# Kernel tuning notes

Measured on AMD Instinct MI355X. Metric: run time of the kernel, lower is better.

Reference implementation:

```python
import jax, jax.numpy as jnp
import numpy as np

B, T, D_MODEL, N_HEAD = 2, 2048, 1024, 16
HEAD_DIM = D_MODEL // N_HEAD
CHUNK, POLY = 16, 1
SCALE = HEAD_DIM ** -0.5


def alpert_basis(L):
    # poly_order=1: constant + linear Legendre-like columns, L2-normalized per column
    t = jnp.linspace(-1.0, 1.0, L)
    W = jnp.stack([jnp.ones_like(t), t], axis=1)  # [L, 2]
    return W / jnp.linalg.norm(W, axis=0, keepdims=True)


def setup_inputs() -> dict:
    key = jax.random.key(0)
    ks = jax.random.split(key, 10)
    d = D_MODEL
    nrm = lambda k, shape, s=0.02: (jax.random.normal(k, shape, jnp.float32) * s)
    return {
        'x': jax.random.normal(ks[0], (B, T, d), jnp.float32),
        'Wq': nrm(ks[1], (d, d)),
        'Wk': nrm(ks[2], (d, d)),
        'Wv': nrm(ks[3], (d, d)),
        'Wo': nrm(ks[4], (d, d)),
        'gate_w': nrm(ks[5], (d, d)),
        'gate_b': jnp.zeros((d,), jnp.float32),
        'A': nrm(ks[6], (N_HEAD, HEAD_DIM, HEAD_DIM)),
        'jump_scale': jnp.ones((1,), jnp.float32),
        'jump_bias': jnp.zeros((1,), jnp.float32),
        'sink_scalar': nrm(ks[7], (1, N_HEAD, 1, 1)),
        'v_null': nrm(ks[8], (1, N_HEAD, 1, HEAD_DIM)),
    }


def _forward(x, Wq, Wk, Wv, Wo, gate_w, gate_b, A, jump_scale, jump_bias, sink_scalar, v_null):
    Bx, Tx, C = x.shape
    H, Dh = N_HEAD, HEAD_DIM
    NEG = jnp.float32(-1e30)

    def lin(W):  # torch Linear: y = x @ W.T, W is [out, in]
        y = jnp.einsum('btc,dc->btd', x, W)
        return y.reshape(Bx, Tx, H, Dh).transpose(0, 2, 1, 3)  # [B,H,T,Dh]

    q_raw, k_raw, v_val = lin(Wq), lin(Wk), lin(Wv)
    g = jax.nn.sigmoid(jnp.einsum('btc,dc->btd', x, gate_w) + gate_b)
    gate = g.reshape(Bx, Tx, H, Dh).transpose(0, 2, 1, 3)

    # symmetric mean/std normalization (torch std is unbiased -> ddof=1)
    ms = 0.5 * (q_raw.mean(-1, keepdims=True) + k_raw.mean(-1, keepdims=True))
    ss = 0.5 * (jnp.std(q_raw, -1, keepdims=True, ddof=1) + jnp.std(k_raw, -1, keepdims=True, ddof=1))
    q_norm = (q_raw - ms) / (ss + 1e-6)
    k_norm = (k_raw - ms) / (ss + 1e-6)

    # RoPE (half-split variant as in source)
    inv = 1.0 / (10000.0 ** (jnp.arange(0, Dh, 2, dtype=jnp.float32) / Dh))
    fr = jnp.arange(Tx, dtype=jnp.float32)[:, None] * inv[None, :]  # [T, Dh/2]
    cos, sin = jnp.cos(fr)[None, None], jnp.sin(fr)[None, None]

    def rope(z):
        z1, z2 = z[..., 0::2], z[..., 1::2]
        return jnp.concatenate([-z2 * sin + z1 * cos, z1 * sin + z2 * cos], axis=-1)

    S = A - jnp.swapaxes(A, -1, -2)  # skew-symmetric per head
    wedge = lambda z: z + jnp.einsum('bhtd,hde->bhte', z, S)
    q_geo, k_geo = wedge(rope(q_norm)), wedge(rope(k_norm))

    W_b = alpert_basis(CHUNK)  # [L, K]
    N, K, L = Tx // CHUNK, W_b.shape[1], CHUNK
    to_chunks = lambda z: z.reshape(Bx, H, N, L, Dh).transpose(2, 0, 1, 3, 4)  # [N,B,H,L,Dh]
    qx, kx, gx = to_chunks(q_geo), to_chunks(k_geo), to_chunks(gate)

    hist0 = jnp.zeros((Bx, H, N, K, Dh), jnp.float32)
    last0 = jnp.zeros((Bx, H, 1, Dh), jnp.float32)
    idx = jnp.arange(N)

    def step(carry, xs):
        hist, last, i = carry
        q_c, k_c, g_c = xs  # [B,H,L,Dh]
        k_coef = jnp.einsum('bhld,lk->bhkd', k_c, W_b)
        sc = jnp.einsum('bhkd,bhnkd->bhn', k_coef, hist) * SCALE
        sc = jnp.where(idx < i, sc, NEG)  # mask unfilled history slots
        w = jax.nn.softmax(sc, axis=-1)
        retr = jnp.einsum('bhn,bhnkd->bhkd', w, hist)
        q_rec = jnp.einsum('bhkd,lk->bhld', retr, W_b)
        jg = jax.nn.sigmoid(sc.max(-1)[..., None, None] * jump_scale + jump_bias)  # [B,H,1,1]
        inj = jnp.where(i > 0, (1.0 - jg) * last + jg * q_rec, 0.0)
        q_out = jnp.cumsum(g_c * q_c, axis=2) + inj
        hist = hist.at[:, :, i].set(jnp.einsum('bhld,lk->bhkd', q_out, W_b))
        return (hist, q_out[:, :, -1:, :], i + 1), q_out

    _, q_outs = jax.lax.scan(step, (hist0, last0, jnp.int32(0)), (qx, kx, gx))
    Q = q_outs.transpose(1, 2, 0, 3, 4).reshape(Bx, H, Tx, Dh)

    att = jnp.einsum('bhtd,bhsd->bhts', Q, k_geo) * SCALE
    causal = jnp.tril(jnp.ones((Tx, Tx), bool))
    att = jnp.where(causal, att, NEG)
    null = jnp.broadcast_to(sink_scalar, (Bx, H, Tx, 1))
    probs = jax.nn.softmax(jnp.concatenate([att, null], axis=-1), axis=-1)
    out = jnp.einsum('bhts,bhsd->bhtd', probs[..., :Tx], v_val) + probs[..., Tx:] * v_null
    out = out.transpose(0, 2, 1, 3).reshape(Bx, Tx, C)
    return jnp.einsum('btc,dc->btd', out, Wo)


def reference(x, Wq, Wk, Wv, Wo, gate_w, gate_b, A, jump_scale, jump_bias, sink_scalar, v_null):
    return _forward(x, Wq, Wk, Wv, Wo, gate_w, gate_b, A, jump_scale, jump_bias, sink_scalar, v_null)
```

## Files before the change

### kernel.cpp

```cpp
#include <hip/hip_runtime.h>
#include <math.h>

#define NB 2
#define NT 2048
#define NH 16
#define DH 64
#define DM 1024

using bf8   = __attribute__((ext_vector_type(8))) short;
using f32x4 = __attribute__((ext_vector_type(4))) float;

static __device__ __forceinline__ ushort f2bf(float f) {
    union { float f; unsigned u; } c; c.f = f;
    unsigned u = c.u + 0x7FFFu + ((c.u >> 16) & 1u);
    return (ushort)(u >> 16);
}

static __device__ __forceinline__ float wbf(int l, int k) {
    if (k == 0) return 0.25f;
    const float invn = 1.0f / sqrtf(1360.0f / 225.0f);
    return (-1.0f + (2.0f / 15.0f) * (float)l) * invn;
}

__global__ __launch_bounds__(256) void cast3_kernel(
    const float* __restrict__ x, const float* __restrict__ wv,
    const float* __restrict__ wo, ushort* __restrict__ xb, ushort* __restrict__ wb)
{
    const int id = blockIdx.x * 256 + threadIdx.x;
    const int XQ = (NB * NT * DM) / 4;
    const int WQ = (DM * DM) / 4;
    const float4* src;
    ushort* dst;
    if (id < XQ) {
        src = (const float4*)x + id;
        dst = xb + (size_t)id * 4;
    } else {
        const int r = id - XQ;
        const int wi = r / WQ, off = r % WQ;
        const float* w = (wi == 0) ? wv : wo;
        src = (const float4*)w + off;
        dst = wb + (size_t)wi * DM * DM + (size_t)off * 4;
    }
    const float4 v = *src;
    ushort4 o;
    o.x = f2bf(v.x); o.y = f2bf(v.y); o.z = f2bf(v.z); o.w = f2bf(v.w);
    *(ushort4*)dst = o;
}

__global__ __launch_bounds__(512) void gemm3_f32_kernel(
    const float* __restrict__ x, const float* __restrict__ Wq,
    const float* __restrict__ Wk, const float* __restrict__ gw,
    const float* __restrict__ gbias,
    float* __restrict__ oq, float* __restrict__ ok, float* __restrict__ og)
{
    __shared__ float As[16][132];
    __shared__ float Bs[16][132];
    const int z = blockIdx.z;
    const float* Bw = (z == 0) ? Wq : (z == 1) ? Wk : gw;
    float* C = (z == 0) ? oq : (z == 1) ? ok : og;
    const int tid = threadIdx.x;
    const int tx = tid & 31;
    const int ty = tid >> 5;
    const int row0 = blockIdx.y * 128, col0 = blockIdx.x * 128;
    const int sr = tid >> 2;
    const int sk = (tid & 3) << 2;
    const float* Ap = x  + (size_t)(row0 + sr) * DM + sk;
    const float* Bp = Bw + (size_t)(col0 + sr) * DM + sk;
    float acc[8][4] = {};
    for (int k0 = 0; k0 < DM; k0 += 16) {
        const float4 av = *(const float4*)(Ap + k0);
        const float4 bv = *(const float4*)(Bp + k0);
        __syncthreads();
        As[sk + 0][sr] = av.x; As[sk + 1][sr] = av.y; As[sk + 2][sr] = av.z; As[sk + 3][sr] = av.w;
        Bs[sk + 0][sr] = bv.x; Bs[sk + 1][sr] = bv.y; Bs[sk + 2][sr] = bv.z; Bs[sk + 3][sr] = bv.w;
        __syncthreads();
        #pragma unroll
        for (int kk = 0; kk < 16; ++kk) {
            const float4 a0 = *(const float4*)&As[kk][ty * 4];
            const float4 a1 = *(const float4*)&As[kk][64 + ty * 4];
            const float4 b0 = *(const float4*)&Bs[kk][tx * 4];
            const float a[8] = {a0.x, a0.y, a0.z, a0.w, a1.x, a1.y, a1.z, a1.w};
            const float b[4] = {b0.x, b0.y, b0.z, b0.w};
            #pragma unroll
            for (int i = 0; i < 8; ++i)
                #pragma unroll
                for (int j = 0; j < 4; ++j)
                    acc[i][j] = fmaf(a[i], b[j], acc[i][j]);
        }
    }
    #pragma unroll
    for (int i = 0; i < 8; ++i) {
        const int m = row0 + ((i < 4) ? (ty * 4 + i) : (64 + ty * 4 + i - 4));
        const int bb = m >> 11, t = m & 2047;
        #pragma unroll
        for (int j = 0; j < 4; ++j) {
            const int n = col0 + tx * 4 + j;
            float v = acc[i][j];
            if (z == 2) v = 1.0f / (1.0f + __expf(-(v + gbias[n])));
            const int h = n >> 6, dh = n & 63;
            C[(((size_t)(bb * NH + h)) * NT + t) * DH + dh] = v;
        }
    }
}

__global__ __launch_bounds__(256) void gemm_bf16_kernel(
    const ushort* __restrict__ Ab, const ushort* __restrict__ Bb,
    float* __restrict__ Cp)
{
    __shared__ ushort Al[128][40];
    __shared__ ushort Bl[64][40];
    const int tid = threadIdx.x;
    const int l = tid & 63, w = tid >> 6;
    const int wr = w >> 1, wc = w & 1;
    const int lr = l & 15, g = l >> 4;
    const int row0 = blockIdx.y * 128, col0 = blockIdx.x * 64;
    f32x4 acc[4][2];
    #pragma unroll
    for (int mi = 0; mi < 4; ++mi)
        #pragma unroll
        for (int ni = 0; ni < 2; ++ni) acc[mi][ni] = (f32x4){0.f, 0.f, 0.f, 0.f};
    const int sa_row = tid >> 1, sa_half = (tid & 1) * 16;
    const int sb_row = tid >> 2, sb_q = (tid & 3) * 8;
    const ushort* Ap = Ab + (size_t)(row0 + sa_row) * DM + sa_half;
    const ushort* Bp = Bb + (size_t)(col0 + sb_row) * DM + sb_q;
    for (int k0 = 0; k0 < DM; k0 += 32) {
        const uint4 a0 = *(const uint4*)(Ap + k0);
        const uint4 a1 = *(const uint4*)(Ap + k0 + 8);
        const uint4 b0 = *(const uint4*)(Bp + k0);
        __syncthreads();
        *(uint4*)&Al[sa_row][sa_half]     = a0;
        *(uint4*)&Al[sa_row][sa_half + 8] = a1;
        *(uint4*)&Bl[sb_row][sb_q]        = b0;
        __syncthreads();
        bf8 a[4], b[2];
        #pragma unroll
        for (int mi = 0; mi < 4; ++mi) a[mi] = *(const bf8*)&Al[wr * 64 + mi * 16 + lr][g * 8];
        #pragma unroll
        for (int ni = 0; ni < 2; ++ni) b[ni] = *(const bf8*)&Bl[wc * 32 + ni * 16 + lr][g * 8];
        #pragma unroll
        for (int mi = 0; mi < 4; ++mi)
            #pragma unroll
            for (int ni = 0; ni < 2; ++ni)
                acc[mi][ni] = __builtin_amdgcn_mfma_f32_16x16x32_bf16(a[mi], b[ni], acc[mi][ni], 0, 0, 0);
    }
    #pragma unroll
    for (int mi = 0; mi < 4; ++mi) {
        const int m0 = row0 + wr * 64 + mi * 16 + g * 4;
        #pragma unroll
        for (int ni = 0; ni < 2; ++ni) {
            const int n = col0 + wc * 32 + ni * 16 + lr;
            #pragma unroll
            for (int r = 0; r < 4; ++r)
                Cp[(size_t)(m0 + r) * DM + n] = acc[mi][ni][r];
        }
    }
}

__global__ __launch_bounds__(256) void nrw_kernel(
    const float* __restrict__ qraw, const float* __restrict__ kraw,
    const float* __restrict__ Amat, float* __restrict__ gateq,
    ushort* __restrict__ kgb,
    float* __restrict__ kcoefA, float* __restrict__ R0A,
    float* __restrict__ R1A, float* __restrict__ r15A)
{
    __shared__ float S[64][64];
    __shared__ float zq[4][64];
    __shared__ float zk[4][64];
    const int bh = blockIdx.x;
    const int h = bh & (NH - 1);
    const int tid = threadIdx.x;
    const int g = tid >> 6, lane = tid & 63;
    for (int idx = tid; idx < 4096; idx += 256) {
        const int d = idx >> 6, e = idx & 63;
        S[d][e] = Amat[(size_t)h * 4096 + d * 64 + e] - Amat[(size_t)h * 4096 + e * 64 + d];
    }
    __syncthreads();
    const int j = lane & 31;
    const float invf = powf(10000.0f, -(float)(2 * j) * (1.0f / 64.0f));
    const int t0 = blockIdx.y * 64 + g * 16;
    float kc0 = 0.f, kc1 = 0.f, run = 0.f, Ra0 = 0.f, Ra1 = 0.f;
    for (int r = 0; r < 16; ++r) {
        const int t = t0 + r;
        const size_t base = ((size_t)bh * NT + t) * DH;
        const float qv = qraw[base + lane];
        const float kv = kraw[base + lane];
        float sq = qv, sk = kv, qq = qv * qv, kk2 = kv * kv;
        #pragma unroll
        for (int off = 32; off; off >>= 1) {
            sq += __shfl_xor(sq, off);
            sk += __shfl_xor(sk, off);
            qq += __shfl_xor(qq, off);
            kk2 += __shfl_xor(kk2, off);
        }
        const float mq = sq * (1.0f / 64.0f), mk = sk * (1.0f / 64.0f);
        const float vq = (qq - 64.0f * mq * mq) * (1.0f / 63.0f);
        const float vk = (kk2 - 64.0f * mk * mk) * (1.0f / 63.0f);
        const float ms = 0.5f * (mq + mk);
        const float ss = 0.5f * (sqrtf(fmaxf(vq, 0.0f)) + sqrtf(fmaxf(vk, 0.0f)));
        const float rinv = 1.0f / (ss + 1e-6f);
        const float qn = (qv - ms) * rinv;
        const float kn = (kv - ms) * rinv;
        const float q1 = __shfl(qn, 2 * j), q2 = __shfl(qn, 2 * j + 1);
        const float k1 = __shfl(kn, 2 * j), k2 = __shfl(kn, 2 * j + 1);
        float sn, cs;
        sincosf((float)t * invf, &sn, &cs);
        const float rq = (lane < 32) ? (q1 * cs - q2 * sn) : (q1 * sn + q2 * cs);
        const float rk = (lane < 32) ? (k1 * cs - k2 * sn) : (k1 * sn + k2 * cs);
        zq[g][lane] = rq;
        zk[g][lane] = rk;
        float aq = 0.0f, ak = 0.0f;
        #pragma unroll 8
        for (int d = 0; d < 64; ++d) {
            const float sde = S[d][lane];
            aq = fmaf(zq[g][d], sde, aq);
            ak = fmaf(zk[g][d], sde, ak);
        }
        const float qgv = rq + aq;
        const float kgv = rk + ak;
        const float gv = gateq[base + lane];
        const float qgpv = gv * qgv;
        gateq[base + lane] = qgpv;
        kgb[base + lane] = f2bf(kgv);
        kc0 = fmaf(kgv, 0.25f, kc0);
        kc1 = fmaf(kgv, wbf(r, 1), kc1);
        run += qgpv;
        Ra0 = fmaf(run, 0.25f, Ra0);
        Ra1 = fmaf(run, wbf(r, 1), Ra1);
    }
    const int unit = bh * 128 + blockIdx.y * 4 + g;
    kcoefA[(size_t)unit * 128 + lane] = kc0;
    kcoefA[(size_t)unit * 128 + 64 + lane] = kc1;
    R0A[(size_t)unit * 64 + lane] = Ra0;
    R1A[(size_t)unit * 64 + lane] = Ra1;
    r15A[(size_t)unit * 64 + lane] = run;
}

__global__ __launch_bounds__(256) void scan_vgemm_kernel(
    const float* __restrict__ kcoefA, const float* __restrict__ R0A,
    const float* __restrict__ R1A, const float* __restrict__ r15A,
    const float* __restrict__ jscale, const float* __restrict__ jbias,
    float* __restrict__ r0O, float* __restrict__ r1O,
    float* __restrict__ lpO, float* __restrict__ jgO,
    const ushort* __restrict__ xb, const ushort* __restrict__ Wb,
    ushort* __restrict__ Vt)
{
    __shared__ char smem[100864];
    if (blockIdx.x >= 32) {
        const int gi = blockIdx.x - 32;
        const int col0 = (gi & 15) * 64;
        const int row0 = (gi >> 4) * 128;
        ushort (*Al)[40] = (ushort(*)[40])smem;
        ushort (*Bl)[40] = (ushort(*)[40])(smem + 10240);
        const int tid = threadIdx.x;
        const int l = tid & 63, w = tid >> 6;
        const int wr = w >> 1, wc = w & 1;
        const int lr = l & 15, g = l >> 4;
        f32x4 acc[4][2];
        #pragma unroll
        for (int mi = 0; mi < 4; ++mi)
            #pragma unroll
            for (int ni = 0; ni < 2; ++ni) acc[mi][ni] = (f32x4){0.f, 0.f, 0.f, 0.f};
        const int sa_row = tid >> 1, sa_half = (tid & 1) * 16;
        const int sb_row = tid >> 2, sb_q = (tid & 3) * 8;
        const ushort* Ap = xb + (size_t)(row0 + sa_row) * DM + sa_half;
        const ushort* Bp = Wb + (size_t)(col0 + sb_row) * DM + sb_q;
        for (int k0 = 0; k0 < DM; k0 += 32) {
            const uint4 a0 = *(const uint4*)(Ap + k0);
            const uint4 a1 = *(const uint4*)(Ap + k0 + 8);
            const uint4 b0 = *(const uint4*)(Bp + k0);
            __syncthreads();
            *(uint4*)&Al[sa_row][sa_half]     = a0;
            *(uint4*)&Al[sa_row][sa_half + 8] = a1;
            *(uint4*)&Bl[sb_row][sb_q]        = b0;
            __syncthreads();
            bf8 a[4], b[2];
            #pragma unroll
            for (int mi = 0; mi < 4; ++mi) a[mi] = *(const bf8*)&Al[wr * 64 + mi * 16 + lr][g * 8];
            #pragma unroll
            for (int ni = 0; ni < 2; ++ni) b[ni] = *(const bf8*)&Bl[wc * 32 + ni * 16 + lr][g * 8];
            #pragma unroll
            for (int mi = 0; mi < 4; ++mi)
                #pragma unroll
                for (int ni = 0; ni < 2; ++ni)
                    acc[mi][ni] = __builtin_amdgcn_mfma_f32_16x16x32_bf16(a[mi], b[ni], acc[mi][ni], 0, 0, 0);
        }
        #pragma unroll
        for (int mi = 0; mi < 4; ++mi) {
            const int m0 = row0 + wr * 64 + mi * 16 + g * 4;
            const int bb = m0 >> 11, t0 = m0 & 2047;
            #pragma unroll
            for (int ni = 0; ni < 2; ++ni) {
                const int n = col0 + wc * 32 + ni * 16 + lr;
                const int h = n >> 6, dh = n & 63;
                ushort4 pk;
                pk.x = f2bf(acc[mi][ni][0]); pk.y = f2bf(acc[mi][ni][1]);
                pk.z = f2bf(acc[mi][ni][2]); pk.w = f2bf(acc[mi][ni][3]);
                *(ushort4*)(Vt + (((size_t)(bb * NH + h)) * DH + dh) * NT + t0) = pk;
            }
        }
        return;
    }
    if (threadIdx.x >= 64) return;
    float* HA  = (float*)smem;
    float* KcL = (float*)(smem + 65536);
    float* EL  = (float*)(smem + 73728);
    float* ET  = (float*)(smem + 82176);
    float* VP  = (float*)(smem + 92416);
    float* mxold = (float*)(smem + 100608);
    float* psold = (float*)(smem + 100672);
    float* pbuf  = (float*)(smem + 100736);
    const int bh = blockIdx.x;
    const int l = threadIdx.x;
    #pragma unroll
    for (int c = 0; c < 64; ++c)
        *(f32x4*)&HA[c * 256 + l * 4] = (f32x4){0.f, 0.f, 0.f, 0.f};
    const float js = jscale[0], jb = jbias[0];
    const float* kcp  = kcoefA + (size_t)bh * 128 * 128;
    const float* R0p  = R0A  + (size_t)bh * 128 * 64;
    const float* R1p  = R1A  + (size_t)bh * 128 * 64;
    const float* r15p = r15A + (size_t)bh * 128 * 64;
    float* r0o = r0O + (size_t)bh * 128 * 64;
    float* r1o = r1O + (size_t)bh * 128 * 64;
    float* lpo = lpO + (size_t)bh * 128 * 64;
    float* jgo = jgO + (size_t)bh * 128;
    float last = 0.0f;
    const float wb15_1 = wbf(15, 1);
    const int iiq = l >> 2, sq = l & 3;
    const int ch = l >> 2;

    for (int j = 0; j < 8; ++j) {
        const int P = 16 * j;
        #pragma unroll
        for (int t = 0; t < 8; ++t)
            *(f32x4*)&KcL[t * 256 + l * 4] = *(const f32x4*)&kcp[j * 2048 + t * 256 + l * 4];
        float R0b[16], R1b[16], r15b[16];
        #pragma unroll
        for (int t = 0; t < 16; ++t) {
            R0b[t]  = R0p[(P + t) * 64 + l];
            R1b[t]  = R1p[(P + t) * 64 + l];
            r15b[t] = r15p[(P + t) * 64 + l];
        }
        {
            float sA[16], sB[16];
            #pragma unroll
            for (int ii = 0; ii < 16; ++ii) { sA[ii] = 0.f; sB[ii] = 0.f; }
            const int swA = l & 31;
            for (int c = 0; c < 32; ++c) {
                const int cs = ((c ^ swA) << 2);
                const f32x4 hA = *(const f32x4*)&HA[l * 128 + cs];
                const f32x4 hB = *(const f32x4*)&HA[(64 + l) * 128 + cs];
                #pragma unroll
                for (int ii = 0; ii < 16; ++ii) {
                    const f32x4 kc = *(const f32x4*)&KcL[ii * 128 + (c << 2)];
                    sA[ii] = fmaf(hA[0], kc[0], sA[ii]); sA[ii] = fmaf(hA[1], kc[1], sA[ii]);
                    sA[ii] = fmaf(hA[2], kc[2], sA[ii]); sA[ii] = fmaf(hA[3], kc[3], sA[ii]);
                    sB[ii] = fmaf(hB[0], kc[0], sB[ii]); sB[ii] = fmaf(hB[1], kc[1], sB[ii]);
                    sB[ii] = fmaf(hB[2], kc[2], sB[ii]); sB[ii] = fmaf(hB[3], kc[3], sB[ii]);
                }
            }
            #pragma unroll
            for (int ii = 0; ii < 16; ++ii) {
                if (l < P)      EL[ii * 132 + l]      = sA[ii] * 0.125f;
                if (64 + l < P) EL[ii * 132 + 64 + l] = sB[ii] * 0.125f;
            }
        }
        {
            float m = -1e30f;
            for (int n = sq; n < P; n += 4) m = fmaxf(m, EL[iiq * 132 + n]);
            m = fmaxf(m, __shfl_xor(m, 1));
            m = fmaxf(m, __shfl_xor(m, 2));
            if (sq == 0) mxold[iiq] = m;
        }
        {
            const float mo = (P > 0) ? mxold[iiq] : -1e30f;
            float ps = 0.f;
            for (int n = sq; n < P; n += 4) {
                const float e = __expf(EL[iiq * 132 + n] - mo);
                ET[n * 20 + iiq] = e;
                ps += e;
            }
            ps += __shfl_xor(ps, 1);
            ps += __shfl_xor(ps, 2);
            if (sq == 0) psold[iiq] = ps;
        }
        {
            float vp0[16], vp1[16];
            #pragma unroll
            for (int ii = 0; ii < 16; ++ii) { vp0[ii] = 0.f; vp1[ii] = 0.f; }
            for (int n = 0; n < P; ++n) {
                const int sw = n & 31;
                const float h0 = HA[n * 128 + ((ch ^ sw) << 2) + (l & 3)];
                const float h1 = HA[n * 128 + (((16 + ch) ^ sw) << 2) + (l & 3)];
                const f32x4 e0 = *(const f32x4*)&ET[n * 20];
                const f32x4 e1 = *(const f32x4*)&ET[n * 20 + 4];
                const f32x4 e2 = *(const f32x4*)&ET[n * 20 + 8];
                const f32x4 e3 = *(const f32x4*)&ET[n * 20 + 12];
                #pragma unroll
                for (int u = 0; u < 4; ++u) {
                    vp0[u]      = fmaf(e0[u], h0, vp0[u]);      vp1[u]      = fmaf(e0[u], h1, vp1[u]);
                    vp0[4 + u]  = fmaf(e1[u], h0, vp0[4 + u]);  vp1[4 + u]  = fmaf(e1[u], h1, vp1[4 + u]);
                    vp0[8 + u]  = fmaf(e2[u], h0, vp0[8 + u]);  vp1[8 + u]  = fmaf(e2[u], h1, vp1[8 + u]);
                    vp0[12 + u] = fmaf(e3[u], h0, vp0[12 + u]); vp1[12 + u] = fmaf(e3[u], h1, vp1[12 + u]);
                }
            }
            #pragma unroll
            for (int ii = 0; ii < 16; ++ii) {
                VP[ii * 128 + l]      = vp0[ii];
                VP[ii * 128 + 64 + l] = vp1[ii];
            }
        }
        const int n_ = l >> 2, q = l & 3;
        #pragma unroll
        for (int iL = 0; iL < 16; ++iL) {
            const int i = P + iL;
            const int nrow = P + n_;
            const int nsw = nrow & 31;
            float scn = 0.f;
            #pragma unroll
            for (int c = 0; c < 8; ++c) {
                const f32x4 h  = *(const f32x4*)&HA[nrow * 128 + ((((q << 3) + c) ^ nsw) << 2)];
                const f32x4 kc = *(const f32x4*)&KcL[iL * 128 + (q << 5) + (c << 2)];
                scn = fmaf(h[0], kc[0], scn); scn = fmaf(h[1], kc[1], scn);
                scn = fmaf(h[2], kc[2], scn); scn = fmaf(h[3], kc[3], scn);
            }
            scn += __shfl_xor(scn, 1);
            scn += __shfl_xor(scn, 2);
            const float cand = (n_ < iL) ? scn * 0.125f : -1e30f;
            float mxn = cand;
            mxn = fmaxf(mxn, __shfl_xor(mxn, 4));
            mxn = fmaxf(mxn, __shfl_xor(mxn, 8));
            mxn = fmaxf(mxn, __shfl_xor(mxn, 16));
            mxn = fmaxf(mxn, __shfl_xor(mxn, 32));
            const float mo = mxold[iL];
            const float mx = fmaxf(mxn, mo);
            const float p = (n_ < iL) ? __expf(cand - mx) : 0.f;
            float psn = p;
            psn += __shfl_xor(psn, 4);
            psn += __shfl_xor(psn, 8);
            psn += __shfl_xor(psn, 16);
            psn += __shfl_xor(psn, 32);
            if (q == 0) pbuf[n_] = p;
            float r0 = 0.f, r1 = 0.f;
            if (i > 0) {
                const float so = __expf(mo - mx);
                float racc0 = VP[iL * 128 + l] * so;
                float racc1 = VP[iL * 128 + 64 + l] * so;
                #pragma unroll
                for (int n2 = 0; n2 < iL; ++n2) {
                    const float pn = pbuf[n2];
                    const int nr = P + n2;
                    const int sw2 = nr & 31;
                    racc0 = fmaf(pn, HA[nr * 128 + ((ch ^ sw2) << 2) + (l & 3)], racc0);
                    racc1 = fmaf(pn, HA[nr * 128 + (((16 + ch) ^ sw2) << 2) + (l & 3)], racc1);
                }
                const float ps = fmaf(psold[iL], so, psn);
                const float rden = 1.0f / ps;
                r0 = racc0 * rden;
                r1 = racc1 * rden;
            }
            const float jg = 1.0f / (1.0f + __expf(-fmaf(mx, js, jb)));
            const float lastp = last;
            const float h0n = R0b[iL] + fmaf(jg, r0, 4.0f * (1.0f - jg) * lastp);
            const float h1n = fmaf(jg, r1, R1b[iL]);
            const float qrec15 = fmaf(r0, 0.25f, r1 * wb15_1);
            last = r15b[iL] + fmaf(jg, qrec15, (1.0f - jg) * lastp);
            r0o[i * 64 + l] = r0;
            r1o[i * 64 + l] = r1;
            lpo[i * 64 + l] = lastp;
            if (l == 0) jgo[i] = jg;
            const int swi = i & 31;
            HA[i * 128 + ((ch ^ swi) << 2) + (l & 3)] = h0n;
            HA[i * 128 + (((16 + ch) ^ swi) << 2) + (l & 3)] = h1n;
        }
    }
}

__global__ __launch_bounds__(256) void scan_post_kernel(
    const float* __restrict__ qgp, const float* __restrict__ r0O,
    const float* __restrict__ r1O, const float* __restrict__ lpO,
    const float* __restrict__ jgO, float* __restrict__ Qout)
{
    const int unit = blockIdx.x * 4 + (threadIdx.x >> 6);
    const int d = threadIdx.x & 63;
    const int bh = unit >> 7, i = unit & 127;
    const size_t ub = (size_t)unit * 64 + d;
    const float r0 = r0O[ub], r1 = r1O[ub], lp = lpO[ub];
    const float jg = jgO[unit];
    const size_t cbase = ((size_t)bh * NT + i * 16) * DH + d;
    float run = 0.0f;
    #pragma unroll
    for (int ll = 0; ll < 16; ++ll) {
        run += qgp[cbase + ll * 64];
        const float qrec = fmaf(r0, 0.25f, r1 * wbf(ll, 1));
        const float inj = (i > 0) ? fmaf(jg, qrec, (1.0f - jg) * lp) : 0.0f;
        Qout[cbase + ll * 64] = run + inj;
    }
}

__global__ __launch_bounds__(256) void attn_mfma_kernel(
    const float* __restrict__ Qf, const ushort* __restrict__ Kb,
    const ushort* __restrict__ Vtb, const float* __restrict__ sink,
    const float* __restrict__ vnull, ushort* __restrict__ Ob)
{
    __shared__ ushort Kl0[64][40], Kl1[64][40];
    __shared__ ushort Vl0[64][40], Vl1[64][40];
    __shared__ ushort Pl[4][2][16][40];
    const int bh = blockIdx.y;
    const int h = bh & (NH - 1);
    const int b = bh >> 4;
    const int qt = gridDim.x - 1 - blockIdx.x;
    const int q0 = qt * 64;
    const int tid = threadIdx.x;
    const int w = tid >> 6, l = tid & 63;
    const int lr = l & 15, g = l >> 4;
    bf8 qf[2];
    {
        const float* qp = Qf + (((size_t)bh * NT) + q0 + 16 * w + lr) * DH + g * 8;
        #pragma unroll
        for (int ks = 0; ks < 2; ++ks) {
            const float4 f0 = *(const float4*)(qp + 32 * ks);
            const float4 f1 = *(const float4*)(qp + 32 * ks + 4);
            bf8 q;
            q[0] = (short)f2bf(f0.x); q[1] = (short)f2bf(f0.y);
            q[2] = (short)f2bf(f0.z); q[3] = (short)f2bf(f0.w);
            q[4] = (short)f2bf(f1.x); q[5] = (short)f2bf(f1.y);
            q[6] = (short)f2bf(f1.z); q[7] = (short)f2bf(f1.w);
            qf[ks] = q;
        }
    }
    f32x4 oacc[4];
    #pragma unroll
    for (int nf2 = 0; nf2 < 4; ++nf2) oacc[nf2] = (f32x4){0.f, 0.f, 0.f, 0.f};
    float mrow[4], lrowp[4];
    #pragma unroll
    for (int r = 0; r < 4; ++r) { mrow[r] = -1e30f; lrowp[r] = 0.0f; }
    const int ntiles = qt + 1;
    const ushort* Kg = Kb + (size_t)bh * NT * DH;
    const ushort* Vg = Vtb + (size_t)bh * DH * NT;
    const int srow = tid >> 2;
    const int sc16 = (tid & 3) * 16;
    for (int it = 0; it < ntiles; ++it) {
        const int kv0 = it * 64;
        __syncthreads();
        {
            const ushort* kp = Kg + (size_t)(kv0 + srow) * DH + sc16;
            const ushort* vp = Vg + (size_t)srow * NT + kv0 + sc16;
            ushort* kd = (sc16 < 32) ? &Kl0[srow][sc16] : &Kl1[srow][sc16 - 32];
            ushort* vd = (sc16 < 32) ? &Vl0[srow][sc16] : &Vl1[srow][sc16 - 32];
            *(uint4*)kd       = *(const uint4*)kp;
            *(uint4*)(kd + 8) = *(const uint4*)(kp + 8);
            *(uint4*)vd       = *(const uint4*)vp;
            *(uint4*)(vd + 8) = *(const uint4*)(vp + 8);
        }
        __syncthreads();
        f32x4 s[4];
        #pragma unroll
        for (int nf = 0; nf < 4; ++nf) {
            s[nf] = (f32x4){0.f, 0.f, 0.f, 0.f};
            const bf8 kf0 = *(const bf8*)&Kl0[nf * 16 + lr][g * 8];
            const bf8 kf1 = *(const bf8*)&Kl1[nf * 16 + lr][g * 8];
            s[nf] = __builtin_amdgcn_mfma_f32_16x16x32_bf16(qf[0], kf0, s[nf], 0, 0, 0);
            s[nf] = __builtin_amdgcn_mfma_f32_16x16x32_bf16(qf[1], kf1, s[nf], 0, 0, 0);
        }
        #pragma unroll
        for (int r = 0; r < 4; ++r) {
            const int row = q0 + 16 * w + g * 4 + r;
            float sv[4];
            float tmax = -1e30f;
            #pragma unroll
            for (int nf = 0; nf < 4; ++nf) {
                const int col = kv0 + nf * 16 + lr;
                sv[nf] = (col <= row) ? s[nf][r] * 0.125f : -1e30f;
                tmax = fmaxf(tmax, sv[nf]);
            }
            tmax = fmaxf(tmax, __shfl_xor(tmax, 1));
            tmax = fmaxf(tmax, __shfl_xor(tmax, 2));
            tmax = fmaxf(tmax, __shfl_xor(tmax, 4));
            tmax = fmaxf(tmax, __shfl_xor(tmax, 8));
            const float mnew = fmaxf(mrow[r], tmax);
            const float csc = __expf(mrow[r] - mnew);
            float plocal = 0.f;
            #pragma unroll
            for (int nf = 0; nf < 4; ++nf) {
                const float p = __expf(sv[nf] - mnew);
                plocal += p;
                Pl[w][nf >> 1][g * 4 + r][(nf & 1) * 16 + lr] = f2bf(p);
            }
            lrowp[r] = lrowp[r] * csc + plocal;
            mrow[r] = mnew;
            #pragma unroll
            for (int nf2 = 0; nf2 < 4; ++nf2) oacc[nf2][r] *= csc;
        }
        const bf8 pa0 = *(const bf8*)&Pl[w][0][lr][g * 8];
        const bf8 pa1 = *(const bf8*)&Pl[w][1][lr][g * 8];
        #pragma unroll
        for (int nf2 = 0; nf2 < 4; ++nf2) {
            const bf8 vb0 = *(const bf8*)&Vl0[nf2 * 16 + lr][g * 8];
            const bf8 vb1 = *(const bf8*)&Vl1[nf2 * 16 + lr][g * 8];
            oacc[nf2] = __builtin_amdgcn_mfma_f32_16x16x32_bf16(pa0, vb0, oacc[nf2], 0, 0, 0);
            oacc[nf2] = __builtin_amdgcn_mfma_f32_16x16x32_bf16(pa1, vb1, oacc[nf2], 0, 0, 0);
        }
    }
    float lrow[4];
    #pragma unroll
    for (int r = 0; r < 4; ++r) {
        float ps = lrowp[r];
        ps += __shfl_xor(ps, 1);
        ps += __shfl_xor(ps, 2);
        ps += __shfl_xor(ps, 4);
        ps += __shfl_xor(ps, 8);
        lrow[r] = ps;
    }
    const float s0 = sink[h];
    float c0v[4], pnv[4], rden[4];
    #pragma unroll
    for (int r = 0; r < 4; ++r) {
        const float mf = fmaxf(mrow[r], s0);
        c0v[r] = __expf(mrow[r] - mf);
        pnv[r] = __expf(s0 - mf);
        rden[r] = 1.0f / fmaf(lrow[r], c0v[r], pnv[r]);
    }
    #pragma unroll
    for (int nf2 = 0; nf2 < 4; ++nf2) {
        const float vn = vnull[h * DH + nf2 * 16 + lr];
        #pragma unroll
        for (int r = 0; r < 4; ++r) {
            const float out = fmaf(pnv[r], vn, oacc[nf2][r] * c0v[r]) * rden[r];
            const int trow = q0 + 16 * w + g * 4 + r;
            Ob[(((size_t)b * NT) + trow) * DM + h * DH + nf2 * 16 + lr] = f2bf(out);
        }
    }
}

extern "C" void kernel_launch(void* const* d_in, const int* in_sizes, int n_in,
                              void* d_out, int out_size, void* d_ws, size_t ws_size,
                              hipStream_t stream) {
    const float* x     = (const float*)d_in[0];
    const float* Wq    = (const float*)d_in[1];
    const float* Wk    = (const float*)d_in[2];
    const float* Wv    = (const float*)d_in[3];
    const float* Wo    = (const float*)d_in[4];
    const float* gw    = (const float*)d_in[5];
    const float* gbias = (const float*)d_in[6];
    const float* Amat  = (const float*)d_in[7];
    const float* js    = (const float*)d_in[8];
    const float* jb    = (const float*)d_in[9];
    const float* sink  = (const float*)d_in[10];
    const float* vnull = (const float*)d_in[11];
    char* ws = (char*)d_ws;
    const size_t MB = 1024 * 1024;
    float*  q_raw  = (float*)(ws + 0);
    float*  k_raw  = (float*)(ws + 16 * MB);
    float*  gate   = (float*)(ws + 32 * MB);
    ushort* kgb    = (ushort*)(ws + 64 * MB);
    ushort* xb     = (ushort*)(ws + 72 * MB);
    ushort* Wb     = (ushort*)(ws + 80 * MB);
    float*  kcoefA = (float*)(ws + 84 * MB);
    float*  R0A    = (float*)(ws + 86 * MB);
    float*  R1A    = (float*)(ws + 87 * MB);
    float*  r15A   = (float*)(ws + 88 * MB);
    float*  r0O    = (float*)(ws + 89 * MB);
    float*  r1O    = (float*)(ws + 90 * MB);
    float*  lpO    = (float*)(ws + 91 * MB);
    float*  jgO    = (float*)(ws + 92 * MB);
    ushort* Vt     = (ushort*)k_raw;
    ushort* attob  = (ushort*)(ws + 24 * MB);

    cast3_kernel<<<6144, 256, 0, stream>>>(x, Wv, Wo, xb, Wb);
    gemm3_f32_kernel<<<dim3(DM / 128, (NB * NT) / 128, 3), 512, 0, stream>>>(
        x, Wq, Wk, gw, gbias, q_raw, k_raw, gate);
    nrw_kernel<<<dim3(NB * NH, NT / 64), 256, 0, stream>>>(
        q_raw, k_raw, Amat, gate, kgb, kcoefA, R0A, R1A, r15A);
    scan_vgemm_kernel<<<32 + 512, 256, 0, stream>>>(
        kcoefA, R0A, R1A, r15A, js, jb, r0O, r1O, lpO, jgO, xb, Wb, Vt);
    scan_post_kernel<<<1024, 256, 0, stream>>>(gate, r0O, r1O, lpO, jgO, q_raw);
    attn_mfma_kernel<<<dim3(NT / 64, NB * NH), 256, 0, stream>>>(q_raw, kgb, Vt, sink, vnull, attob);
    gemm_bf16_kernel<<<dim3(DM / 64, (NB * NT) / 128), 256, 0, stream>>>(
        attob, Wb + DM * DM, (float*)d_out);
}
```

Baseline: 808.2 us.

## Fuse bf16 cast into f32 GEMM launch and use LDS reductions in scan

Merges the cast kernel into the fp32 QKG GEMM launch as extra trailing blocks on a flattened 1-D grid, removing one kernel launch and letting the cast overlap with the GEMM. In the sequential scan loop, the cross-lane shuffle reductions for score sum, max and exp-sum are replaced with writes to shared memory followed by every lane reading and reducing the 16 values. This trades shuffle latency for LDS traffic and relies on single-wavefront lockstep with no explicit barriers. The new qbuf/candBuf alias a region of the scan's shared memory that must be free at that point.

```diff
diff --git a/kernel.cpp b/kernel.cpp
--- a/kernel.cpp
+++ b/kernel.cpp
@@ -22,46 +22,48 @@
     return (-1.0f + (2.0f / 15.0f) * (float)l) * invn;
 }
 
-__global__ __launch_bounds__(256) void cast3_kernel(
-    const float* __restrict__ x, const float* __restrict__ wv,
-    const float* __restrict__ wo, ushort* __restrict__ xb, ushort* __restrict__ wb)
-{
-    const int id = blockIdx.x * 256 + threadIdx.x;
-    const int XQ = (NB * NT * DM) / 4;
-    const int WQ = (DM * DM) / 4;
-    const float4* src;
-    ushort* dst;
-    if (id < XQ) {
-        src = (const float4*)x + id;
-        dst = xb + (size_t)id * 4;
-    } else {
-        const int r = id - XQ;
-        const int wi = r / WQ, off = r % WQ;
-        const float* w = (wi == 0) ? wv : wo;
-        src = (const float4*)w + off;
-        dst = wb + (size_t)wi * DM * DM + (size_t)off * 4;
-    }
-    const float4 v = *src;
-    ushort4 o;
-    o.x = f2bf(v.x); o.y = f2bf(v.y); o.z = f2bf(v.z); o.w = f2bf(v.w);
-    *(ushort4*)dst = o;
-}
-
-__global__ __launch_bounds__(512) void gemm3_f32_kernel(
+__global__ __launch_bounds__(512) void gemm3c_kernel(
     const float* __restrict__ x, const float* __restrict__ Wq,
     const float* __restrict__ Wk, const float* __restrict__ gw,
     const float* __restrict__ gbias,
-    float* __restrict__ oq, float* __restrict__ ok, float* __restrict__ og)
+    float* __restrict__ oq, float* __restrict__ ok, float* __restrict__ og,
+    const float* __restrict__ wv, const float* __restrict__ wo,
+    ushort* __restrict__ xb, ushort* __restrict__ wb)
 {
     __shared__ float As[16][132];
     __shared__ float Bs[16][132];
-    const int z = blockIdx.z;
+    if (blockIdx.x >= 768) {
+        const int id = (blockIdx.x - 768) * 512 + threadIdx.x;
+        const int XQ = (NB * NT * DM) / 4;
+        const int WQ = (DM * DM) / 4;
+        const float4* src;
+        ushort* dst;
+        if (id < XQ) {
+            src = (const float4*)x + id;
+            dst = xb + (size_t)id * 4;
+        } else {
+            const int r = id - XQ;
+            const int wi = r / WQ, off = r % WQ;
+            const float* w = (wi == 0) ? wv : wo;
+            src = (const float4*)w + off;
+            dst = wb + (size_t)wi * DM * DM + (size_t)off * 4;
+        }
+        const float4 v = *src;
+        ushort4 o;
+        o.x = f2bf(v.x); o.y = f2bf(v.y); o.z = f2bf(v.z); o.w = f2bf(v.w);
+        *(ushort4*)dst = o;
+        return;
+    }
+    const int b = blockIdx.x;
+    const int z = b >> 8;
+    const int by = (b >> 3) & 31;
+    const int bx = b & 7;
     const float* Bw = (z == 0) ? Wq : (z == 1) ? Wk : gw;
     float* C = (z == 0) ? oq : (z == 1) ? ok : og;
     const int tid = threadIdx.x;
     const int tx = tid & 31;
     const int ty = tid >> 5;
-    const int row0 = blockIdx.y * 128, col0 = blockIdx.x * 128;
+    const int row0 = by * 128, col0 = bx * 128;
     const int sr = tid >> 2;
     const int sk = (tid & 3) << 2;
     const float* Ap = x  + (size_t)(row0 + sr) * DM + sk;
@@ -80,12 +82,12 @@
             const float4 a1 = *(const float4*)&As[kk][64 + ty * 4];
             const float4 b0 = *(const float4*)&Bs[kk][tx * 4];
             const float a[8] = {a0.x, a0.y, a0.z, a0.w, a1.x, a1.y, a1.z, a1.w};
-            const float b[4] = {b0.x, b0.y, b0.z, b0.w};
+            const float bb2[4] = {b0.x, b0.y, b0.z, b0.w};
             #pragma unroll
             for (int i = 0; i < 8; ++i)
                 #pragma unroll
                 for (int j = 0; j < 4; ++j)
-                    acc[i][j] = fmaf(a[i], b[j], acc[i][j]);
+                    acc[i][j] = fmaf(a[i], bb2[j], acc[i][j]);
         }
     }
     #pragma unroll
@@ -309,6 +311,8 @@
     float* mxold = (float*)(smem + 100608);
     float* psold = (float*)(smem + 100672);
     float* pbuf  = (float*)(smem + 100736);
+    float* qbuf    = (float*)(smem + 73728);
+    float* candBuf = (float*)(smem + 74752);
     const int bh = blockIdx.x;
     const int l = threadIdx.x;
     #pragma unroll
@@ -410,36 +414,40 @@
             }
         }
         const int n_ = l >> 2, q = l & 3;
+        const int qb = l & ~3;
         #pragma unroll
         for (int iL = 0; iL < 16; ++iL) {
             const int i = P + iL;
             const int nrow = P + n_;
             const int nsw = nrow & 31;
-            float scn = 0.f;
+            float scp = 0.f;
             #pragma unroll
             for (int c = 0; c < 8; ++c) {
                 const f32x4 h  = *(const f32x4*)&HA[nrow * 128 + ((((q << 3) + c) ^ nsw) << 2)];
                 const f32x4 kc = *(const f32x4*)&KcL[iL * 128 + (q << 5) + (c << 2)];
-                scn = fmaf(h[0], kc[0], scn); scn = fmaf(h[1], kc[1], scn);
-                scn = fmaf(h[2], kc[2], scn); scn = fmaf(h[3], kc[3], scn);
-            }
-            scn += __shfl_xor(scn, 1);
-            scn += __shfl_xor(scn, 2);
+                scp = fmaf(h[0], kc[0], scp); scp = fmaf(h[1], kc[1], scp);
+                scp = fmaf(h[2], kc[2], scp); scp = fmaf(h[3], kc[3], scp);
+            }
+            qbuf[l] = scp;
+            const float scn = (qbuf[qb] + qbuf[qb + 1]) + (qbuf[qb + 2] + qbuf[qb + 3]);
             const float cand = (n_ < iL) ? scn * 0.125f : -1e30f;
-            float mxn = cand;
-            mxn = fmaxf(mxn, __shfl_xor(mxn, 4));
-            mxn = fmaxf(mxn, __shfl_xor(mxn, 8));
-            mxn = fmaxf(mxn, __shfl_xor(mxn, 16));
-            mxn = fmaxf(mxn, __shfl_xor(mxn, 32));
+            if (q == 0) candBuf[n_] = cand;
+            float m8[8];
+            #pragma unroll
+            for (int u = 0; u < 8; ++u) m8[u] = fmaxf(candBuf[2 * u], candBuf[2 * u + 1]);
+            float m4a = fmaxf(m8[0], m8[1]), m4b = fmaxf(m8[2], m8[3]);
+            float m4c = fmaxf(m8[4], m8[5]), m4d = fmaxf(m8[6], m8[7]);
+            const float mxn = fmaxf(fmaxf(m4a, m4b), fmaxf(m4c, m4d));
             const float mo = mxold[iL];
             const float mx = fmaxf(mxn, mo);
             const float p = (n_ < iL) ? __expf(cand - mx) : 0.f;
-            float psn = p;
-            psn += __shfl_xor(psn, 4);
-            psn += __shfl_xor(psn, 8);
-            psn += __shfl_xor(psn, 16);
-            psn += __shfl_xor(psn, 32);
             if (q == 0) pbuf[n_] = p;
+            float s8[8];
+            #pragma unroll
+            for (int u = 0; u < 8; ++u) s8[u] = pbuf[2 * u] + pbuf[2 * u + 1];
+            float s4a = s8[0] + s8[1], s4b = s8[2] + s8[3];
+            float s4c = s8[4] + s8[5], s4d = s8[6] + s8[7];
+            const float psn = (s4a + s4b) + (s4c + s4d);
             float r0 = 0.f, r1 = 0.f;
             if (i > 0) {
                 const float so = __expf(mo - mx);
@@ -666,9 +674,8 @@
     ushort* Vt     = (ushort*)k_raw;
     ushort* attob  = (ushort*)(ws + 24 * MB);
 
-    cast3_kernel<<<6144, 256, 0, stream>>>(x, Wv, Wo, xb, Wb);
-    gemm3_f32_kernel<<<dim3(DM / 128, (NB * NT) / 128, 3), 512, 0, stream>>>(
-        x, Wq, Wk, gw, gbias, q_raw, k_raw, gate);
+    gemm3c_kernel<<<3840, 512, 0, stream>>>(
+        x, Wq, Wk, gw, gbias, q_raw, k_raw, gate, Wv, Wo, xb, Wb);
     nrw_kernel<<<dim3(NB * NH, NT / 64), 256, 0, stream>>>(
         q_raw, k_raw, Amat, gate, kgb, kcoefA, R0A, R1A, r15A);
     scan_vgemm_kernel<<<32 + 512, 256, 0, stream>>>(
```

Result: no change. 797.6 us, median of 2 (-1.3%).
